# Performance work log

Measured on AMD Instinct MI355X. Metric: run time of the kernel, lower is better.

The kernel has to match this reference:

```python
import jax, jax.numpy as jnp
import numpy as np

B, L, D, H, DFF = 2, 2048, 1024, 16, 4096
DH = D // H  # 64
EPS = 1e-6


def setup_inputs() -> dict:
    key = jax.random.key(0)
    ks = jax.random.split(key, 12)
    s = 0.02  # weight init scale
    inp = {
        "x": jax.random.normal(ks[0], (B, L, D), jnp.float32),
        "Wq": jax.random.normal(ks[1], (D, D), jnp.float32) * s,
        "bq": jnp.zeros((D,), jnp.float32),
        "Wk": jax.random.normal(ks[2], (D, D), jnp.float32) * s,
        "bk": jnp.zeros((D,), jnp.float32),
        "Wv": jax.random.normal(ks[3], (D, D), jnp.float32) * s,
        "bv": jnp.zeros((D,), jnp.float32),
        "Wo": jax.random.normal(ks[4], (D, D), jnp.float32) * s,
        "bo": jnp.zeros((D,), jnp.float32),
        "E": jax.random.normal(ks[5], (L, DH), jnp.float32),  # max_seq==L rel. embeddings
        "W1": jax.random.normal(ks[6], (D, DFF), jnp.float32) * s,
        "b1": jnp.zeros((DFF,), jnp.float32),
        "W2": jax.random.normal(ks[7], (DFF, D), jnp.float32) * s,
        "b2": jnp.zeros((D,), jnp.float32),
        "g1": jnp.ones((D,), jnp.float32),
        "beta1": jnp.zeros((D,), jnp.float32),
        "g2": jnp.ones((D,), jnp.float32),
        "beta2": jnp.zeros((D,), jnp.float32),
    }
    return inp


def _layernorm(x, g, b):
    mu = jnp.mean(x, axis=-1, keepdims=True)
    var = jnp.mean(jnp.square(x - mu), axis=-1, keepdims=True)
    return (x - mu) * jax.lax.rsqrt(var + EPS) * g + b


def _qe_mask(qe):
    # keep entries where col j >= len_k - 1 - row i (upper-right triangle)
    lq, lk = qe.shape[-2], qe.shape[-1]
    keep = jnp.arange(lk)[None, :] >= (lk - 1 - jnp.arange(lq))[:, None]
    return qe * keep.astype(qe.dtype)


def _skew(qe):
    # Music-Transformer skewing: pad 1 on the left of last dim, reshape, drop first row
    b, h, lq, lk = qe.shape
    padded = jnp.pad(qe, ((0, 0), (0, 0), (0, 0), (1, 0)))  # [b,h,lq,lk+1]
    reshaped = padded.reshape(b, h, lk + 1, lq)
    return reshaped[:, :, 1:, :]  # [b,h,lk,lq] == [b,h,lq,lk] since lq==lk here


def reference(x, Wq, bq, Wk, bk, Wv, bv, Wo, bo, E, W1, b1, W2, b2, g1, beta1, g2, beta2):
    b, l, d = x.shape
    # projections -> [b, h, l, dh]
    def split_heads(t):
        return t.reshape(b, l, H, DH).transpose(0, 2, 1, 3)

    q = split_heads(x @ Wq + bq)
    k = split_heads(x @ Wk + bk)
    v = split_heads(x @ Wv + bv)

    # relative logits: E sliced to last len_q rows (len_q == max_seq here -> all of E)
    e = E[E.shape[0] - l:, :]  # [l, dh]
    qe = jnp.einsum("bhld,md->bhlm", q, e)
    srel = _skew(_qe_mask(qe))  # [b,h,l,l]

    logits = (jnp.einsum("bhld,bhmd->bhlm", q, k) + srel) / np.sqrt(DH).astype(np.float32)
    attn = jax.nn.softmax(logits, axis=-1)
    out = jnp.einsum("bhlm,bhmd->bhld", attn, v)
    out = out.transpose(0, 2, 1, 3).reshape(b, l, d)
    attn_out = out @ Wo + bo

    out1 = _layernorm(attn_out + x, g1, beta1)
    ffn = jax.nn.relu(out1 @ W1 + b1) @ W2 + b2
    out2 = _layernorm(out1 + ffn, g2, beta2)
    return out2
```

## Files before the change

### kernel.cpp

```cpp
#include <hip/hip_runtime.h>

typedef unsigned short u16;
typedef __attribute__((ext_vector_type(8))) short s16x8;
typedef __attribute__((ext_vector_type(4))) float f32x4;

#define MFMA16(a,b,c) __builtin_amdgcn_mfma_f32_16x16x32_bf16((a),(b),(c),0,0,0)
#define LSEQ 2048
#define QSCALE 0.18033688011112042f

__device__ __forceinline__ u16 f2b(float f) {
  union { float f; unsigned u; } v; v.f = f;
  unsigned r = v.u + 0x7FFFu + ((v.u >> 16) & 1u);
  return (u16)(r >> 16);
}
__device__ __forceinline__ void g2l16(const void* g, void* l) {
  __builtin_amdgcn_global_load_lds(
      (const __attribute__((address_space(1))) unsigned int*)g,
      (__attribute__((address_space(3))) unsigned int*)l, 16, 0, 0);
}

__global__ __launch_bounds__(256) void k_prep_all(
    const float* __restrict__ x, const float* __restrict__ E,
    const float* __restrict__ bq, const float* __restrict__ bk, const float* __restrict__ bv,
    const float* __restrict__ Wq, const float* __restrict__ Wk, const float* __restrict__ Wv,
    const float* __restrict__ Wo, const float* __restrict__ W1, const float* __restrict__ W2,
    u16* __restrict__ xb, u16* __restrict__ Ebf, float* __restrict__ bcat,
    u16* __restrict__ Wqt, u16* __restrict__ Wot, u16* __restrict__ W1t, u16* __restrict__ W2t) {
  __shared__ float T[64][65];
  const int b = blockIdx.x, tid = threadIdx.x;

  if (b < 1056) {
    const float* src = (b < 1024) ? x : E;
    u16* dst = (b < 1024) ? xb : Ebf;
    const int base = (b < 1024) ? b * 4096 : (b - 1024) * 4096;
#pragma unroll
    for (int p = 0; p < 4; p++) {
      int i = base + p * 1024 + tid * 4;
      float4 v = *(const float4*)(src + i);
      ushort4 o;
      o.x = f2b(v.x); o.y = f2b(v.y); o.z = f2b(v.z); o.w = f2b(v.w);
      *(ushort4*)(dst + i) = o;
    }
    return;
  }
  if (b == 1056) {
    for (int i = tid; i < 3072; i += 256)
      bcat[i] = (i < 1024) ? bq[i] : (i < 2048) ? bk[i - 1024] : bv[i - 2048];
    return;
  }

  const int idx = b - 1057;
  const float* W; u16* Wt; int K, N, bx, by;
  if (idx < 1024) {
    const int m = idx >> 8, ti = idx & 255;
    const float* ws4[4] = {Wq, Wk, Wv, Wo};
    W = ws4[m];
    Wt = (m < 3) ? (Wqt + (size_t)m * 1048576) : Wot;
    K = 1024; N = 1024; bx = ti & 15; by = ti >> 4;
  } else if (idx < 2048) {
    const int ti = idx - 1024;
    W = W1; Wt = W1t; K = 1024; N = 4096; bx = ti & 63; by = ti >> 6;
  } else {
    const int ti = idx - 2048;
    W = W2; Wt = W2t; K = 4096; N = 1024; bx = ti & 15; by = ti >> 4;
  }
  const int k0 = by * 64, n0 = bx * 64;
  const int r = tid >> 4, c4 = (tid & 15) * 4;
#pragma unroll
  for (int i = 0; i < 4; i++) {
    float4 v = *(const float4*)(W + (size_t)(k0 + r + i * 16) * N + n0 + c4);
    T[r + i * 16][c4 + 0] = v.x; T[r + i * 16][c4 + 1] = v.y;
    T[r + i * 16][c4 + 2] = v.z; T[r + i * 16][c4 + 3] = v.w;
  }
  __syncthreads();
#pragma unroll
  for (int i = 0; i < 4; i++) {
    int nl = r + i * 16;
    ushort4 o;
    o.x = f2b(T[c4 + 0][nl]); o.y = f2b(T[c4 + 1][nl]);
    o.z = f2b(T[c4 + 2][nl]); o.w = f2b(T[c4 + 3][nl]);
    *(ushort4*)(Wt + (size_t)(n0 + nl) * K + k0 + c4) = o;
  }
}

template <int BM, int BN, int FLAGS, int BK>
__global__ __launch_bounds__(BM == 256 ? 512 : 256, BM == 256 ? 4 : 2)
void k_gemm(const u16* __restrict__ A, const u16* __restrict__ Bt,
            const float* __restrict__ bias, const void* __restrict__ resid,
            void* __restrict__ Cout, int M, int N, int K) {
  constexpr int MI = (BN == 128) ? 4 : 2;
  constexpr int KH = BK / 32;
  __shared__ __align__(16) u16 As[2][KH][BM * 32];
  __shared__ __align__(16) u16 Bs[2][KH][BN * 32];
  const int tid = threadIdx.x;
  const int lane = tid & 63, wave = tid >> 6;
  const int lo = lane & 15, hi = lane >> 4;
  const int WROW = (BN == 128) ? (wave >> 1) * 64 : wave * 32;
  const int WCOL = (BN == 128) ? (wave & 1) * 64 : 0;
  const int m0 = blockIdx.y * BM, n0 = blockIdx.x * BN;

  const int colg = ((lane & 3) * 16) ^ (((lane >> 3) & 3) << 4);
  const int arow = wave * 32 + (lane >> 2);
  const int swzr = ((lane >> 1) & 3) << 4;

  f32x4 acc[MI][4];
#pragma unroll
  for (int mi = 0; mi < MI; mi++)
#pragma unroll
    for (int ni = 0; ni < 4; ni++) acc[mi][ni] = (f32x4){0.f, 0.f, 0.f, 0.f};

  const char* Ab = (const char*)A;
  const char* Bb = (const char*)Bt;
  const int nt = K / BK;

  auto stage = [&](int buf, int t) {
#pragma unroll
    for (int h = 0; h < KH; h++) {
      const int k0 = t * BK + h * 32;
      char* ad = (char*)&As[buf][h][0] + wave * 2048;
      const char* as = Ab + ((size_t)(m0 + arow) * K + k0) * 2 + colg;
      g2l16(as, ad);
      g2l16(as + (size_t)16 * K * 2, ad + 1024);
      if (BM == 256) {
        char* bd = (char*)&Bs[buf][h][0] + wave * 1024;
        const char* bs = Bb + ((size_t)(n0 + wave * 16 + (lane >> 2)) * K + k0) * 2 + colg;
        g2l16(bs, bd);
      } else if (BN == 128) {
        char* bd = (char*)&Bs[buf][h][0] + wave * 2048;
        const char* bs = Bb + ((size_t)(n0 + arow) * K + k0) * 2 + colg;
        g2l16(bs, bd);
        g2l16(bs + (size_t)16 * K * 2, bd + 1024);
      } else {
        char* bd = (char*)&Bs[buf][h][0] + wave * 1024;
        const int brow = wave * 16 + (lane >> 2);
        const char* bs = Bb + ((size_t)(n0 + brow) * K + k0) * 2 + colg;
        g2l16(bs, bd);
      }
    }
  };

  stage(0, 0);
  int buf = 0;
  for (int t = 0; t < nt; t++) {
    __syncthreads();
    if (t + 1 < nt) stage(buf ^ 1, t + 1);
#pragma unroll
    for (int h = 0; h < KH; h++) {
      const char* ab = (const char*)&As[buf][h][0];
      const char* bb2 = (const char*)&Bs[buf][h][0];
      s16x8 af[MI], bfr[4];
#pragma unroll
      for (int mi = 0; mi < MI; mi++) {
        int row = WROW + mi * 16 + lo;
        af[mi] = *(const s16x8*)(ab + row * 64 + ((hi * 16) ^ swzr));
      }
#pragma unroll
      for (int ni = 0; ni < 4; ni++) {
        int row = WCOL + ni * 16 + lo;
        bfr[ni] = *(const s16x8*)(bb2 + row * 64 + ((hi * 16) ^ swzr));
      }
#pragma unroll
      for (int mi = 0; mi < MI; mi++)
#pragma unroll
        for (int ni = 0; ni < 4; ni++)
          acc[mi][ni] = MFMA16(af[mi], bfr[ni], acc[mi][ni]);
    }
    buf ^= 1;
  }

#pragma unroll
  for (int mi = 0; mi < MI; mi++)
#pragma unroll
    for (int ni = 0; ni < 4; ni++) {
      const int mb = m0 + WROW + mi * 16 + hi * 4;
      const int n = n0 + WCOL + ni * 16 + lo;
      float v4[4];
#pragma unroll
      for (int reg = 0; reg < 4; reg++) {
        float v = acc[mi][ni][reg] + bias[n];
        if (FLAGS & 8) v += ((const float*)resid)[(size_t)(mb + reg) * N + n];
        if (FLAGS & 16) {
          union { unsigned u; float f; } q;
          q.u = ((unsigned)((const u16*)resid)[(size_t)(mb + reg) * N + n]) << 16;
          v += q.f;
        }
        if (FLAGS & 1) v = fmaxf(v, 0.f);
        v4[reg] = v;
      }
      if (FLAGS & 4) {
        const int seg = n >> 10, nn = n & 1023;
        const int hh = nn >> 6, dd = nn & 63;
        const int bb = mb >> 11, ll = mb & 2047;
        u16* dst = (u16*)Cout + (size_t)seg * 4194304;
        if (seg == 0) {
#pragma unroll
          for (int reg = 0; reg < 4; reg++)
            dst[((size_t)(bb * 16 + hh) * LSEQ + ll + reg) * 64 + dd] = f2b(v4[reg] * QSCALE);
        } else if (seg == 1) {
#pragma unroll
          for (int reg = 0; reg < 4; reg++)
            dst[((size_t)(bb * 16 + hh) * LSEQ + ll + reg) * 64 + dd] = f2b(v4[reg]);
        } else {
          const int lq = (ll >> 2) & 7;
          const int pq = (lq < 4) ? (lq * 2) : ((lq - 4) * 2 + 1);
          const int llp = (ll & ~31) | (pq << 2);
          ushort4 o;
          o.x = f2b(v4[0]); o.y = f2b(v4[1]); o.z = f2b(v4[2]); o.w = f2b(v4[3]);
          *(ushort4*)&((u16*)dst)[((size_t)(bb * 16 + hh) * 64 + dd) * LSEQ + llp] = o;
        }
      } else if (FLAGS & 2) {
        u16* dst = (u16*)Cout;
#pragma unroll
        for (int reg = 0; reg < 4; reg++) dst[(size_t)(mb + reg) * N + n] = f2b(v4[reg]);
      } else {
        float* dst = (float*)Cout;
#pragma unroll
        for (int reg = 0; reg < 4; reg++) dst[(size_t)(mb + reg) * N + n] = v4[reg];
      }
    }
}

__global__ __launch_bounds__(512, 4) void k_attn(const u16* __restrict__ Qh, const u16* __restrict__ Kh,
                                                 const u16* __restrict__ Vt, const u16* __restrict__ Eb,
                                                 u16* __restrict__ Ob) {
  __shared__ __align__(16) u16 Ksh[2][64 * 64];
  __shared__ __align__(16) u16 Vts[2][64 * 64];
  __shared__ __align__(16) float Gsh[8][16 * 84];

  const int tid = threadIdx.x;
  const int lane = tid & 63, wave = tid >> 6;
  const int lo = lane & 15, hi = lane >> 4;

  const int hb = blockIdx.x;
  const int x = hb & 7;
  const int kk = hb >> 3;
  const int bh = x * 4 + (kk >> 4);
  const int ti = (kk & 32) ? (15 - (kk & 15)) : (kk & 15);
  const int l0 = ti * 128;
  const int bb = bh >> 4, hh = bh & 15;
  const int lw = l0 + wave * 16;

  const u16* Qb = Qh + (size_t)bh * LSEQ * 64;
  const char* Kb = (const char*)(Kh + (size_t)bh * LSEQ * 64);
  const char* Vb = (const char*)(Vt + (size_t)bh * 64 * LSEQ);

  const int colsw = ((lane & 7) * 16) ^ (((lane >> 3) & 7) << 4);
  const int swzv = (lo & 7) << 4;
  const int c0 = (hi * 16) ^ swzv;

  auto stageKV = [&](int buf_, int j0_) {
    char* kd = (char*)&Ksh[buf_][0] + wave * 1024;
    const char* ks = Kb + (size_t)(j0_ + wave * 8 + (lane >> 3)) * 128 + colsw;
    g2l16(ks, kd);
    char* vd = (char*)&Vts[buf_][0] + wave * 1024;
    const char* vs = Vb + (size_t)(wave * 8 + (lane >> 3)) * (LSEQ * 2) + (size_t)j0_ * 2 + colsw;
    g2l16(vs, vd);
  };

  s16x8 aq[2];
  aq[0] = *(const s16x8*)(Qb + (size_t)(lw + lo) * 64 + hi * 8);
  aq[1] = *(const s16x8*)(Qb + (size_t)(lw + lo) * 64 + 32 + hi * 8);

  const s16x8 ones8 = {16256, 16256, 16256, 16256, 16256, 16256, 16256, 16256};

  float m_run = -1e30f, l_run = 0.f;
  f32x4 oacc[4];
#pragma unroll
  for (int f = 0; f < 4; f++) oacc[f] = (f32x4){0.f, 0.f, 0.f, 0.f};

  float* gw = &Gsh[wave][0];

  stageKV(0, 0);
  int buf = 0;

  for (int t = 0; t < 32; t++) {
    const int j0 = t * 64;
    const bool has_rel = (j0 <= lw);
    __syncthreads();
    if (t < 31) stageKV(buf ^ 1, j0 + 64);

    f32x4 s4[4];
#pragma unroll
    for (int c = 0; c < 4; c++) {
      const char* krow = (const char*)&Ksh[buf][0] + (c * 16 + lo) * 128;
      s16x8 a0 = *(const s16x8*)(krow + c0);
      s16x8 a1 = *(const s16x8*)(krow + (c0 ^ 64));
      s4[c] = (f32x4){0.f, 0.f, 0.f, 0.f};
      s4[c] = MFMA16(a0, aq[0], s4[c]);
      s4[c] = MFMA16(a1, aq[1], s4[c]);
    }

    if (has_rel) {
      const int waveBase = 2032 - lw + j0;
      const u16* ep0 = Eb + (size_t)(waveBase + lo) * 64 + hi * 8;
      s16x8 ec0 = *(const s16x8*)(ep0);
      s16x8 ec1 = *(const s16x8*)(ep0 + 32);
#pragma unroll
      for (int c2 = 0; c2 < 5; c2++) {
        s16x8 en0, en1;
        if (c2 < 4) {
          const u16* epn = ep0 + (size_t)(c2 + 1) * 16 * 64;
          en0 = *(const s16x8*)(epn);
          en1 = *(const s16x8*)(epn + 32);
        }
        f32x4 g = (f32x4){0.f, 0.f, 0.f, 0.f};
        g = MFMA16(ec0, aq[0], g);
        g = MFMA16(ec1, aq[1], g);
        *(f32x4*)(gw + 84 * lo + c2 * 16 + 4 * hi) = g;
        if (c2 < 4) { ec0 = en0; ec1 = en1; }
      }
      const int dd = lw - j0;
      if (dd >= 64) {
#pragma unroll
        for (int c = 0; c < 4; c++)
#pragma unroll
          for (int reg = 0; reg < 4; reg++)
            s4[c][reg] += gw[83 * lo + 15 + c * 16 + 4 * hi + reg];
      } else {
        const int rmax = dd + lo;
#pragma unroll
        for (int c = 0; c < 4; c++)
#pragma unroll
          for (int reg = 0; reg < 4; reg++) {
            int jr = c * 16 + 4 * hi + reg;
            float g = gw[83 * lo + 15 + jr];
            s4[c][reg] += (jr <= rmax) ? g : 0.f;
          }
      }
    }

    s16x8 v0f[4], v1f[4];
#pragma unroll
    for (int f = 0; f < 4; f++) {
      const char* vrow = (const char*)&Vts[buf][0] + (f * 16 + lo) * 128;
      v0f[f] = *(const s16x8*)(vrow + c0);
      v1f[f] = *(const s16x8*)(vrow + (c0 ^ 64));
    }

    float mta = fmaxf(fmaxf(fmaxf(s4[0][0], s4[0][1]), fmaxf(s4[0][2], s4[0][3])),
                      fmaxf(fmaxf(s4[1][0], s4[1][1]), fmaxf(s4[1][2], s4[1][3])));
    float mtb = fmaxf(fmaxf(fmaxf(s4[2][0], s4[2][1]), fmaxf(s4[2][2], s4[2][3])),
                      fmaxf(fmaxf(s4[3][0], s4[3][1]), fmaxf(s4[3][2], s4[3][3])));
    float mt = fmaxf(mta, mtb);
    mt = fmaxf(mt, __shfl_xor(mt, 16, 64));
    mt = fmaxf(mt, __shfl_xor(mt, 32, 64));
    if (!__all(mt - m_run <= 8.f)) {
      float mnew = fmaxf(m_run, mt);
      float scl = exp2f(m_run - mnew);
      m_run = mnew;
      l_run *= scl;
#pragma unroll
      for (int f = 0; f < 4; f++)
#pragma unroll
        for (int reg = 0; reg < 4; reg++) oacc[f][reg] *= scl;
    }

    unsigned w8[8];
#pragma unroll
    for (int c = 0; c < 4; c++) {
      float a0 = exp2f(s4[c][0] - m_run), a1 = exp2f(s4[c][1] - m_run);
      float a2 = exp2f(s4[c][2] - m_run), a3 = exp2f(s4[c][3] - m_run);
      asm("v_cvt_pk_bf16_f32 %0, %1, %2" : "=v"(w8[c * 2]) : "v"(a0), "v"(a1));
      asm("v_cvt_pk_bf16_f32 %0, %1, %2" : "=v"(w8[c * 2 + 1]) : "v"(a2), "v"(a3));
    }

    union UU { uint4 u; s16x8 v; };
    UU pb0, pb1;
    pb0.u = make_uint4(w8[0], w8[1], w8[2], w8[3]);
    pb1.u = make_uint4(w8[4], w8[5], w8[6], w8[7]);

    __builtin_amdgcn_s_setprio(1);
    f32x4 ps = (f32x4){0.f, 0.f, 0.f, 0.f};
    ps = MFMA16(ones8, pb0.v, ps);
    ps = MFMA16(ones8, pb1.v, ps);

#pragma unroll
    for (int f = 0; f < 4; f++) {
      oacc[f] = MFMA16(v0f[f], pb0.v, oacc[f]);
      oacc[f] = MFMA16(v1f[f], pb1.v, oacc[f]);
    }
    __builtin_amdgcn_s_setprio(0);

    l_run += ps[0];
    buf ^= 1;
  }

  const float inv = 1.f / l_run;
  const size_t orow = (size_t)(bb * LSEQ + lw + lo) * 1024 + hh * 64;
#pragma unroll
  for (int f = 0; f < 4; f++) {
    ushort4 o;
    o.x = f2b(oacc[f][0] * inv); o.y = f2b(oacc[f][1] * inv);
    o.z = f2b(oacc[f][2] * inv); o.w = f2b(oacc[f][3] * inv);
    *(ushort4*)(Ob + orow + f * 16 + 4 * hi) = o;
  }
}

__global__ __launch_bounds__(256) void k_layernorm(const float* __restrict__ X, const float* __restrict__ gw,
                                                   const float* __restrict__ bw, float* __restrict__ outF,
                                                   u16* __restrict__ outB) {
  __shared__ float red[2][4];
  const int row = blockIdx.x, tid = threadIdx.x;
  const int lane = tid & 63, wave = tid >> 6;
  const float* x = X + (size_t)row * 1024;
  float4 v = *(const float4*)(x + tid * 4);
  float s = v.x + v.y + v.z + v.w;
  float s2 = v.x * v.x + v.y * v.y + v.z * v.z + v.w * v.w;
#pragma unroll
  for (int msk = 1; msk <= 32; msk <<= 1) {
    s += __shfl_xor(s, msk, 64);
    s2 += __shfl_xor(s2, msk, 64);
  }
  if (lane == 0) { red[0][wave] = s; red[1][wave] = s2; }
  __syncthreads();
  s = red[0][0] + red[0][1] + red[0][2] + red[0][3];
  s2 = red[1][0] + red[1][1] + red[1][2] + red[1][3];
  float mean = s * (1.f / 1024.f);
  float var = s2 * (1.f / 1024.f) - mean * mean;
  float rs = rsqrtf(var + 1e-6f);
  float4 g4 = *(const float4*)(gw + tid * 4);
  float4 b4 = *(const float4*)(bw + tid * 4);
  float4 o;
  o.x = (v.x - mean) * rs * g4.x + b4.x;
  o.y = (v.y - mean) * rs * g4.y + b4.y;
  o.z = (v.z - mean) * rs * g4.z + b4.z;
  o.w = (v.w - mean) * rs * g4.w + b4.w;
  if (outF) *(float4*)(outF + (size_t)row * 1024 + tid * 4) = o;
  if (outB) {
    ushort4 ob;
    ob.x = f2b(o.x); ob.y = f2b(o.y); ob.z = f2b(o.z); ob.w = f2b(o.w);
    *(ushort4*)(outB + (size_t)row * 1024 + tid * 4) = ob;
  }
}

extern "C" void kernel_launch(void* const* d_in, const int* in_sizes, int n_in,
                              void* d_out, int out_size, void* d_ws, size_t ws_size,
                              hipStream_t stream) {
  const float* x   = (const float*)d_in[0];
  const float* Wq  = (const float*)d_in[1];
  const float* bq  = (const float*)d_in[2];
  const float* Wk  = (const float*)d_in[3];
  const float* bk  = (const float*)d_in[4];
  const float* Wv  = (const float*)d_in[5];
  const float* bv  = (const float*)d_in[6];
  const float* Wo  = (const float*)d_in[7];
  const float* bo  = (const float*)d_in[8];
  const float* E   = (const float*)d_in[9];
  const float* W1  = (const float*)d_in[10];
  const float* b1  = (const float*)d_in[11];
  const float* W2  = (const float*)d_in[12];
  const float* b2  = (const float*)d_in[13];
  const float* g1  = (const float*)d_in[14];
  const float* be1 = (const float*)d_in[15];
  const float* g2  = (const float*)d_in[16];
  const float* be2 = (const float*)d_in[17];

  char* ws = (char*)d_ws;
  const size_t MB = 1ull << 20;
  u16* Wqt = (u16*)(ws + 0 * MB);
  u16* Wot = (u16*)(ws + 6 * MB);
  u16* W1t = (u16*)(ws + 8 * MB);
  u16* W2t = (u16*)(ws + 16 * MB);
  u16* Ebf = (u16*)(ws + 24 * MB);
  float* bcat = (float*)(ws + 24 * MB + 512 * 1024);
  u16* xb  = (u16*)(ws + 25 * MB);
  u16* qb  = (u16*)(ws + 33 * MB);
  u16* kb  = (u16*)(ws + 41 * MB);
  u16* vt  = (u16*)(ws + 49 * MB);
  u16* ao  = (u16*)(ws + 57 * MB);
  float* t1 = (float*)(ws + 65 * MB);
  u16* o1b  = (u16*)(ws + 25 * MB);
  u16* h1b  = (u16*)(ws + 49 * MB);
  float* outF = (float*)d_out;

  k_prep_all<<<4129, 256, 0, stream>>>(x, E, bq, bk, bv, Wq, Wk, Wv, Wo, W1, W2,
                                       xb, Ebf, bcat, Wqt, Wot, W1t, W2t);

  k_gemm<256, 128, 4, 32><<<dim3(24, 16), 512, 0, stream>>>(xb, Wqt, bcat, nullptr, qb, 4096, 3072, 1024);

  k_attn<<<dim3(512), 512, 0, stream>>>(qb, kb, vt, Ebf, ao);

  k_gemm<128, 64, 8, 64><<<dim3(16, 32), 256, 0, stream>>>(ao, Wot, bo, x, t1, 4096, 1024, 1024);

  k_layernorm<<<4096, 256, 0, stream>>>(t1, g1, be1, nullptr, o1b);

  k_gemm<256, 128, 3, 32><<<dim3(32, 16), 512, 0, stream>>>(o1b, W1t, b1, nullptr, h1b, 4096, 4096, 1024);

  k_gemm<128, 64, 16, 64><<<dim3(16, 32), 256, 0, stream>>>(h1b, W2t, b2, o1b, outF, 4096, 1024, 4096);

  k_layernorm<<<4096, 256, 0, stream>>>(outF, g2, be2, outF, nullptr);
}
```

Before: 309.5 us.

## Shrink attention blocks to four waves and ring-buffer relative-logit staging

```diff
diff --git a/kernel.cpp b/kernel.cpp
--- a/kernel.cpp
+++ b/kernel.cpp
@@ -220,23 +220,21 @@
     }
 }
 
-__global__ __launch_bounds__(512, 4) void k_attn(const u16* __restrict__ Qh, const u16* __restrict__ Kh,
+__global__ __launch_bounds__(256, 4) void k_attn(const u16* __restrict__ Qh, const u16* __restrict__ Kh,
                                                  const u16* __restrict__ Vt, const u16* __restrict__ Eb,
                                                  u16* __restrict__ Ob) {
   __shared__ __align__(16) u16 Ksh[2][64 * 64];
   __shared__ __align__(16) u16 Vts[2][64 * 64];
-  __shared__ __align__(16) float Gsh[8][16 * 84];
+  __shared__ __align__(16) float Gsh[4][16 * 32];
 
   const int tid = threadIdx.x;
   const int lane = tid & 63, wave = tid >> 6;
   const int lo = lane & 15, hi = lane >> 4;
 
   const int hb = blockIdx.x;
-  const int x = hb & 7;
-  const int kk = hb >> 3;
-  const int bh = x * 4 + (kk >> 4);
-  const int ti = (kk & 32) ? (15 - (kk & 15)) : (kk & 15);
-  const int l0 = ti * 128;
+  const int logical = (hb & 7) * 128 + (hb >> 3);
+  const int bh = logical >> 5;
+  const int l0 = (logical & 31) * 64;
   const int bb = bh >> 4, hh = bh & 15;
   const int lw = l0 + wave * 16;
 
@@ -249,12 +247,15 @@
   const int c0 = (hi * 16) ^ swzv;
 
   auto stageKV = [&](int buf_, int j0_) {
-    char* kd = (char*)&Ksh[buf_][0] + wave * 1024;
-    const char* ks = Kb + (size_t)(j0_ + wave * 8 + (lane >> 3)) * 128 + colsw;
-    g2l16(ks, kd);
-    char* vd = (char*)&Vts[buf_][0] + wave * 1024;
-    const char* vs = Vb + (size_t)(wave * 8 + (lane >> 3)) * (LSEQ * 2) + (size_t)j0_ * 2 + colsw;
-    g2l16(vs, vd);
+#pragma unroll
+    for (int i = 0; i < 2; i++) {
+      char* kd = (char*)&Ksh[buf_][0] + wave * 2048 + i * 1024;
+      const char* ks = Kb + (size_t)(j0_ + wave * 16 + i * 8 + (lane >> 3)) * 128 + colsw;
+      g2l16(ks, kd);
+      char* vd = (char*)&Vts[buf_][0] + wave * 2048 + i * 1024;
+      const char* vs = Vb + (size_t)(wave * 16 + i * 8 + (lane >> 3)) * (LSEQ * 2) + (size_t)j0_ * 2 + colsw;
+      g2l16(vs, vd);
+    }
   };
 
   s16x8 aq[2];
@@ -291,6 +292,9 @@
     }
 
     if (has_rel) {
+      const int dd = lw - j0;
+      const bool full = (dd >= 64);
+      const int rmax = dd + lo;
       const int waveBase = 2032 - lw + j0;
       const u16* ep0 = Eb + (size_t)(waveBase + lo) * 64 + hi * 8;
       s16x8 ec0 = *(const s16x8*)(ep0);
@@ -306,26 +310,20 @@
         f32x4 g = (f32x4){0.f, 0.f, 0.f, 0.f};
         g = MFMA16(ec0, aq[0], g);
         g = MFMA16(ec1, aq[1], g);
-        *(f32x4*)(gw + 84 * lo + c2 * 16 + 4 * hi) = g;
-        if (c2 < 4) { ec0 = en0; ec1 = en1; }
-      }
-      const int dd = lw - j0;
-      if (dd >= 64) {
-#pragma unroll
-        for (int c = 0; c < 4; c++)
-#pragma unroll
-          for (int reg = 0; reg < 4; reg++)
-            s4[c][reg] += gw[83 * lo + 15 + c * 16 + 4 * hi + reg];
-      } else {
-        const int rmax = dd + lo;
-#pragma unroll
-        for (int c = 0; c < 4; c++)
+        *(f32x4*)(gw + lo * 32 + (c2 & 1) * 16 + 4 * hi) = g;
+        asm volatile("s_waitcnt lgkmcnt(0)" ::: "memory");
+        __builtin_amdgcn_sched_barrier(0);
+        if (c2 >= 1) {
+          const int c = c2 - 1;
 #pragma unroll
           for (int reg = 0; reg < 4; reg++) {
             int jr = c * 16 + 4 * hi + reg;
-            float g = gw[83 * lo + 15 + jr];
-            s4[c][reg] += (jr <= rmax) ? g : 0.f;
+            int idx = 15 - lo + jr;
+            float gval = gw[lo * 32 + ((idx >> 4) & 1) * 16 + (idx & 15)];
+            s4[c][reg] += (full || jr <= rmax) ? gval : 0.f;
           }
+        }
+        if (c2 < 4) { ec0 = en0; ec1 = en1; }
       }
     }
 
@@ -478,7 +476,7 @@
 
   k_gemm<256, 128, 4, 32><<<dim3(24, 16), 512, 0, stream>>>(xb, Wqt, bcat, nullptr, qb, 4096, 3072, 1024);
 
-  k_attn<<<dim3(512), 512, 0, stream>>>(qb, kb, vt, Ebf, ao);
+  k_attn<<<dim3(1024), 256, 0, stream>>>(qb, kb, vt, Ebf, ao);
 
   k_gemm<128, 64, 8, 64><<<dim3(16, 32), 256, 0, stream>>>(ao, Wot, bo, x, t1, 4096, 1024, 1024);
 
```

Measured after the change: 340.4 us. +10.0%, slower.
